# Performance work log

Hardware: AMD Instinct MI355X
Metric: run time of the kernel (lower is better)

Reference implementation:

```python
import jax, jax.numpy as jnp
import numpy as np

N_NODES = 100000
N_EDGES = 600000
IN_DIM = 128
OUT_DIM = 64


def setup_inputs() -> dict:
    key = jax.random.key(0)
    k1, k2, k3, k4, k5 = jax.random.split(key, 5)
    x = jax.random.normal(k1, (N_NODES, IN_DIM), dtype=jnp.float32)
    edge_index = jax.random.randint(k2, (2, N_EDGES), 0, N_NODES, dtype=jnp.int64)
    edge_weight = jax.random.uniform(k3, (N_EDGES,), dtype=jnp.float32)
    W1 = jax.random.normal(k4, (IN_DIM, IN_DIM), dtype=jnp.float32) / np.sqrt(IN_DIM)
    b1 = jnp.zeros((IN_DIM,), dtype=jnp.float32)
    W2 = jax.random.normal(k5, (IN_DIM, OUT_DIM), dtype=jnp.float32) / np.sqrt(IN_DIM)
    b2 = jnp.zeros((OUT_DIM,), dtype=jnp.float32)
    return {"x": x, "edge_index": edge_index, "edge_weight": edge_weight,
            "W1": W1, "b1": b1, "W2": W2, "b2": b2}


def _spmm(edge_index, edge_weight, h):
    # out[dst] = sum_{e: dst(e)=dst} w_e * h[src(e)]  -- normalized adjacency SpMM
    src, dst = edge_index[0], edge_index[1]
    msg = h[src] * edge_weight[:, None]          # [E, D] gather + scale
    return jax.ops.segment_sum(msg, dst, num_segments=h.shape[0])  # [N, D]


def reference(x, edge_index, edge_weight, W1, b1, W2, b2):
    # Layer 1: GCNConv(in,in) -> ReLU (dropout is identity in eval mode)
    h = _spmm(edge_index, edge_weight, x @ W1) + b1
    h = jax.nn.relu(h)
    # Layer 2: GCNConv(in,out)
    out = _spmm(edge_index, edge_weight, h @ W2) + b2
    return out
```

## Files before the change

kernel.cpp:

```cpp
#include <hip/hip_runtime.h>

#define NN 100000
#define NE 600000
#define DIN 128
#define DOUT 64
#define SCAN_B 256
#define NBLK ((NN + SCAN_B - 1) / SCAN_B)
#define HIST_B ((NE + 255) / 256)
#define PREP_N (DIN * DIN + DIN * DOUT)
#define PREP_B ((PREP_N + 255) / 256)

typedef __attribute__((ext_vector_type(8))) short bf16x8;
typedef __attribute__((ext_vector_type(4))) short s16x4;
typedef __attribute__((ext_vector_type(4))) float f32x4;

__device__ inline short f2bf(float f) {
  union { float f; unsigned u; } v; v.f = f;
  unsigned r = (v.u + 0x7FFF + ((v.u >> 16) & 1)) >> 16;
  return (short)r;
}
__device__ inline float bf2f(unsigned short u) {
  union { unsigned u; float f; } v; v.u = ((unsigned)u) << 16;
  return v.f;
}

__global__ __launch_bounds__(256) void hist_prep_kernel(const int* __restrict__ ei,
                                                        int* __restrict__ cnt,
                                                        const float* __restrict__ W1,
                                                        short* __restrict__ w1t,
                                                        const float* __restrict__ W2,
                                                        short* __restrict__ w2t) {
  const int b = blockIdx.x, t = threadIdx.x;
  if (b < HIST_B) {
    int e = b * 256 + t;
    if (e < NE) atomicAdd(&cnt[ei[NE + e]], 1);
  } else {
    int i = (b - HIST_B) * 256 + t;
    if (i < DIN * DIN) {
      int n = i >> 7, k = i & 127;
      w1t[i] = f2bf(W1[k * DIN + n]);
    } else if (i < PREP_N) {
      int i2 = i - DIN * DIN;
      int n = i2 >> 7, k = i2 & 127;
      w2t[i2] = f2bf(W2[k * DOUT + n]);
    }
  }
}

__global__ __launch_bounds__(256) void scan_local_kernel(const int* __restrict__ cnt,
                                                         int* __restrict__ row_ptr,
                                                         int* __restrict__ blk_sum) {
  __shared__ int s[256];
  const int b = blockIdx.x, t = threadIdx.x;
  const int i = b * 256 + t;
  int v = (i < NN) ? cnt[i] : 0;
  s[t] = v;
  __syncthreads();
  for (int off = 1; off < 256; off <<= 1) {
    int u = (t >= off) ? s[t - off] : 0;
    __syncthreads();
    s[t] += u;
    __syncthreads();
  }
  if (i < NN) row_ptr[i] = s[t] - v;
  if (t == 255) blk_sum[b] = s[255];
}

__global__ __launch_bounds__(512) void scan_blk_kernel(const int* __restrict__ blk_sum,
                                                       int* __restrict__ blk_off) {
  __shared__ int s[512];
  const int t = threadIdx.x;
  int v = (t < NBLK) ? blk_sum[t] : 0;
  s[t] = v;
  __syncthreads();
  for (int off = 1; off < 512; off <<= 1) {
    int u = (t >= off) ? s[t - off] : 0;
    __syncthreads();
    s[t] += u;
    __syncthreads();
  }
  if (t < NBLK) blk_off[t] = s[t] - v;
}

__global__ __launch_bounds__(256) void scan_add_kernel(int* __restrict__ row_ptr,
                                                       const int* __restrict__ blk_off,
                                                       int* __restrict__ next) {
  const int b = blockIdx.x, t = threadIdx.x;
  const int i = b * 256 + t;
  if (i < NN) {
    int v = row_ptr[i] + blk_off[b];
    row_ptr[i] = v;
    next[i] = v;
  }
  if (i == 0) row_ptr[NN] = NE;
}

__global__ __launch_bounds__(256) void scatter_kernel(const int* __restrict__ ei,
                                                      const float* __restrict__ ew,
                                                      int* __restrict__ next,
                                                      int2* __restrict__ ep) {
  int e = blockIdx.x * 256 + threadIdx.x;
  if (e >= NE) return;
  int src = ei[e];
  int dst = ei[NE + e];
  int pos = atomicAdd(&next[dst], 1);
  ep[pos] = make_int2(src, __float_as_int(ew[e]));
}

#define G1_BM 128
#define XS_PITCH 136
__global__ __launch_bounds__(256) void gemm1_mfma_kernel(const float* __restrict__ x,
                                                         const short* __restrict__ w1t,
                                                         short* __restrict__ h0) {
  __shared__ short xs[G1_BM][XS_PITCH];
  const int t = threadIdx.x;
  const int row0 = blockIdx.x * G1_BM;
#pragma unroll
  for (int i = 0; i < 16; ++i) {
    int f = t + i * 256;
    int r = f >> 5, c4 = f & 31;
    int gr = row0 + r;
    float4 v = (gr < NN) ? *(const float4*)&x[(size_t)gr * DIN + c4 * 4]
                         : make_float4(0.f, 0.f, 0.f, 0.f);
    s16x4 s;
    s.x = f2bf(v.x); s.y = f2bf(v.y); s.z = f2bf(v.z); s.w = f2bf(v.w);
    *(s16x4*)&xs[r][c4 * 4] = s;
  }
  __syncthreads();

  const int wave = t >> 6, lane = t & 63;
  const int nlane = lane & 15, quad = lane >> 4;
  const int mbase = wave * 32;
  f32x4 acc[2][8];
#pragma unroll
  for (int mt = 0; mt < 2; ++mt)
#pragma unroll
    for (int nt = 0; nt < 8; ++nt) acc[mt][nt] = (f32x4){0.f, 0.f, 0.f, 0.f};

#pragma unroll
  for (int ks = 0; ks < 4; ++ks) {
    const int koff = ks * 32 + quad * 8;
    bf16x8 a0 = *(const bf16x8*)&xs[mbase + nlane][koff];
    bf16x8 a1 = *(const bf16x8*)&xs[mbase + 16 + nlane][koff];
#pragma unroll
    for (int nt = 0; nt < 8; ++nt) {
      bf16x8 b = *(const bf16x8*)&w1t[(size_t)(nt * 16 + nlane) * DIN + koff];
      acc[0][nt] = __builtin_amdgcn_mfma_f32_16x16x32_bf16(a0, b, acc[0][nt], 0, 0, 0);
      acc[1][nt] = __builtin_amdgcn_mfma_f32_16x16x32_bf16(a1, b, acc[1][nt], 0, 0, 0);
    }
  }

#pragma unroll
  for (int mt = 0; mt < 2; ++mt)
#pragma unroll
    for (int nt = 0; nt < 8; ++nt)
#pragma unroll
      for (int rg = 0; rg < 4; ++rg) {
        int gr = row0 + mbase + mt * 16 + quad * 4 + rg;
        if (gr < NN) h0[(size_t)gr * DIN + nt * 16 + nlane] = f2bf(acc[mt][nt][rg]);
      }
}

__global__ __launch_bounds__(256) void gemm2_mfma_kernel(const short* __restrict__ acc1,
                                                         const float* __restrict__ b1,
                                                         const short* __restrict__ w2t,
                                                         short* __restrict__ h2) {
  __shared__ short xs[G1_BM][XS_PITCH];
  const int t = threadIdx.x;
  const int row0 = blockIdx.x * G1_BM;
#pragma unroll
  for (int i = 0; i < 8; ++i) {
    int f = t + i * 256;
    int r = f >> 4, c8 = f & 15;
    int gr = row0 + r;
    bf16x8 v = (gr < NN) ? *(const bf16x8*)&acc1[(size_t)gr * DIN + c8 * 8]
                         : (bf16x8){0, 0, 0, 0, 0, 0, 0, 0};
    bf16x8 s;
#pragma unroll
    for (int j = 0; j < 8; ++j) {
      float fv = bf2f((unsigned short)v[j]) + b1[c8 * 8 + j];
      s[j] = f2bf(fmaxf(fv, 0.f));
    }
    *(bf16x8*)&xs[r][c8 * 8] = s;
  }
  __syncthreads();

  const int wave = t >> 6, lane = t & 63;
  const int nlane = lane & 15, quad = lane >> 4;
  const int mbase = wave * 32;
  f32x4 acc[2][4];
#pragma unroll
  for (int mt = 0; mt < 2; ++mt)
#pragma unroll
    for (int nt = 0; nt < 4; ++nt) acc[mt][nt] = (f32x4){0.f, 0.f, 0.f, 0.f};

#pragma unroll
  for (int ks = 0; ks < 4; ++ks) {
    const int koff = ks * 32 + quad * 8;
    bf16x8 a0 = *(const bf16x8*)&xs[mbase + nlane][koff];
    bf16x8 a1 = *(const bf16x8*)&xs[mbase + 16 + nlane][koff];
#pragma unroll
    for (int nt = 0; nt < 4; ++nt) {
      bf16x8 b = *(const bf16x8*)&w2t[(size_t)(nt * 16 + nlane) * DIN + koff];
      acc[0][nt] = __builtin_amdgcn_mfma_f32_16x16x32_bf16(a0, b, acc[0][nt], 0, 0, 0);
      acc[1][nt] = __builtin_amdgcn_mfma_f32_16x16x32_bf16(a1, b, acc[1][nt], 0, 0, 0);
    }
  }

#pragma unroll
  for (int mt = 0; mt < 2; ++mt)
#pragma unroll
    for (int nt = 0; nt < 4; ++nt)
#pragma unroll
      for (int rg = 0; rg < 4; ++rg) {
        int gr = row0 + mbase + mt * 16 + quad * 4 + rg;
        if (gr < NN) h2[(size_t)gr * DOUT + nt * 16 + nlane] = f2bf(acc[mt][nt][rg]);
      }
}

template <int D, int LPE, bool BIAS, bool OUTBF>
__global__ __launch_bounds__(256) void spmm_gather_kernel(
    const int* __restrict__ rp, const int2* __restrict__ ep,
    const short* __restrict__ h, const float* __restrict__ bias,
    void* __restrict__ outv) {
  const int row = blockIdx.x * (256 / LPE) + threadIdx.x / LPE;
  const int lane = threadIdx.x % LPE;
  if (row >= NN) return;
  const int b = rp[row], e = rp[row + 1];
  float acc[8];
#pragma unroll
  for (int j = 0; j < 8; ++j) acc[j] = 0.f;
  int i = b;
  for (; i + 4 <= e; i += 4) {
    int2 p0 = ep[i], p1 = ep[i + 1], p2 = ep[i + 2], p3 = ep[i + 3];
    bf16x8 v0 = *(const bf16x8*)&h[(size_t)p0.x * D + lane * 8];
    bf16x8 v1 = *(const bf16x8*)&h[(size_t)p1.x * D + lane * 8];
    bf16x8 v2 = *(const bf16x8*)&h[(size_t)p2.x * D + lane * 8];
    bf16x8 v3 = *(const bf16x8*)&h[(size_t)p3.x * D + lane * 8];
    float w0 = __int_as_float(p0.y), w1 = __int_as_float(p1.y);
    float w2 = __int_as_float(p2.y), w3 = __int_as_float(p3.y);
#pragma unroll
    for (int j = 0; j < 8; ++j)
      acc[j] += w0 * bf2f((unsigned short)v0[j]) + w1 * bf2f((unsigned short)v1[j]) +
                w2 * bf2f((unsigned short)v2[j]) + w3 * bf2f((unsigned short)v3[j]);
  }
  if (i + 2 <= e) {
    int2 p0 = ep[i], p1 = ep[i + 1];
    bf16x8 v0 = *(const bf16x8*)&h[(size_t)p0.x * D + lane * 8];
    bf16x8 v1 = *(const bf16x8*)&h[(size_t)p1.x * D + lane * 8];
    float w0 = __int_as_float(p0.y), w1 = __int_as_float(p1.y);
#pragma unroll
    for (int j = 0; j < 8; ++j)
      acc[j] += w0 * bf2f((unsigned short)v0[j]) + w1 * bf2f((unsigned short)v1[j]);
    i += 2;
  }
  if (i < e) {
    int2 p0 = ep[i];
    bf16x8 v0 = *(const bf16x8*)&h[(size_t)p0.x * D + lane * 8];
    float w0 = __int_as_float(p0.y);
#pragma unroll
    for (int j = 0; j < 8; ++j) acc[j] += w0 * bf2f((unsigned short)v0[j]);
  }
  if (BIAS) {
#pragma unroll
    for (int j = 0; j < 8; ++j) acc[j] += bias[lane * 8 + j];
  }
  if (OUTBF) {
    bf16x8 o;
#pragma unroll
    for (int j = 0; j < 8; ++j) o[j] = f2bf(acc[j]);
    *(bf16x8*)((short*)outv + (size_t)row * D + lane * 8) = o;
  } else {
    float* out = (float*)outv;
    *(float4*)&out[(size_t)row * D + lane * 8] = make_float4(acc[0], acc[1], acc[2], acc[3]);
    *(float4*)&out[(size_t)row * D + lane * 8 + 4] = make_float4(acc[4], acc[5], acc[6], acc[7]);
  }
}

extern "C" void kernel_launch(void* const* d_in, const int* in_sizes, int n_in,
                              void* d_out, int out_size, void* d_ws, size_t ws_size,
                              hipStream_t stream) {
  const float* x  = (const float*)d_in[0];
  const int*   ei = (const int*)d_in[1];
  const float* ew = (const float*)d_in[2];
  const float* W1 = (const float*)d_in[3];
  const float* b1 = (const float*)d_in[4];
  const float* W2 = (const float*)d_in[5];
  const float* b2 = (const float*)d_in[6];
  float* out = (float*)d_out;

  char* p = (char*)d_ws;
  int*   cnt     = (int*)p;                 p += sizeof(int) * NN;
  int*   row_ptr = (int*)p;                 p += sizeof(int) * (NN + 4);
  int*   blk_sum = (int*)p;                 p += sizeof(int) * (NBLK + 1);
  int*   blk_off = (int*)p;                 p += sizeof(int) * (NBLK + 1);
  int2*  ep      = (int2*)p;                p += sizeof(int2) * NE;
  short* w1t     = (short*)p;               p += sizeof(short) * DIN * DIN;
  short* w2t     = (short*)p;               p += sizeof(short) * DIN * DOUT;
  short* h0      = (short*)p;               p += sizeof(short) * (size_t)NN * DIN;
  short* acc1    = (short*)p;
  int*   next    = cnt;
  short* h2      = h0;

  hipMemsetAsync(cnt, 0, sizeof(int) * NN, stream);
  hist_prep_kernel<<<HIST_B + PREP_B, 256, 0, stream>>>(ei, cnt, W1, w1t, W2, w2t);
  scan_local_kernel<<<NBLK, 256, 0, stream>>>(cnt, row_ptr, blk_sum);
  scan_blk_kernel<<<1, 512, 0, stream>>>(blk_sum, blk_off);
  scan_add_kernel<<<NBLK, 256, 0, stream>>>(row_ptr, blk_off, next);
  scatter_kernel<<<HIST_B, 256, 0, stream>>>(ei, ew, next, ep);

  gemm1_mfma_kernel<<<(NN + G1_BM - 1) / G1_BM, 256, 0, stream>>>(x, w1t, h0);
  spmm_gather_kernel<DIN, 16, false, true>
      <<<(NN * 16 + 255) / 256, 256, 0, stream>>>(row_ptr, ep, h0, nullptr, acc1);

  gemm2_mfma_kernel<<<(NN + G1_BM - 1) / G1_BM, 256, 0, stream>>>(acc1, b1, w2t, h2);
  spmm_gather_kernel<DOUT, 8, true, false>
      <<<(NN * 8 + 255) / 256, 256, 0, stream>>>(row_ptr, ep, h2, b2, out);
}
```

Measured before the change: 261.7 us.

## Store layer-1 features in fp8, record atomic ranks, and merge scan kernels

The first GEMM now writes its output as fp8 instead of bf16, and the first SpMM gathers 16 fp8 values per lane. This halves the bytes in the random-gather step. The histogram pass saves each edge's atomic rank so the scatter computes positions directly, with no second atomic pass. The three-kernel scan becomes two kernels of 512-thread blocks, each redoing the small block-sum scan. The fp8 storage adds substantial quantization error to the layer-1 intermediate, which may break accuracy tolerances.

```diff
diff --git a/kernel.cpp b/kernel.cpp
--- a/kernel.cpp
+++ b/kernel.cpp
@@ -4,7 +4,7 @@
 #define NE 600000
 #define DIN 128
 #define DOUT 64
-#define SCAN_B 256
+#define SCAN_B 512
 #define NBLK ((NN + SCAN_B - 1) / SCAN_B)
 #define HIST_B ((NE + 255) / 256)
 #define PREP_N (DIN * DIN + DIN * DOUT)
@@ -13,6 +13,7 @@
 typedef __attribute__((ext_vector_type(8))) short bf16x8;
 typedef __attribute__((ext_vector_type(4))) short s16x4;
 typedef __attribute__((ext_vector_type(4))) float f32x4;
+typedef __attribute__((ext_vector_type(2))) float f32x2;
 
 __device__ inline short f2bf(float f) {
   union { float f; unsigned u; } v; v.f = f;
@@ -23,9 +24,25 @@
   union { unsigned u; float f; } v; v.u = ((unsigned)u) << 16;
   return v.f;
 }
+__device__ inline unsigned char f2fp8(float f) {
+  unsigned pk = __builtin_amdgcn_cvt_pk_fp8_f32(f, f, 0, false);
+  return (unsigned char)(pk & 0xff);
+}
+__device__ inline void fma_fp8x16(uint4 q, float w, float* acc) {
+  f32x2 f;
+  f = __builtin_amdgcn_cvt_pk_f32_fp8(q.x, false); acc[0] += w * f[0];  acc[1] += w * f[1];
+  f = __builtin_amdgcn_cvt_pk_f32_fp8(q.x, true);  acc[2] += w * f[0];  acc[3] += w * f[1];
+  f = __builtin_amdgcn_cvt_pk_f32_fp8(q.y, false); acc[4] += w * f[0];  acc[5] += w * f[1];
+  f = __builtin_amdgcn_cvt_pk_f32_fp8(q.y, true);  acc[6] += w * f[0];  acc[7] += w * f[1];
+  f = __builtin_amdgcn_cvt_pk_f32_fp8(q.z, false); acc[8] += w * f[0];  acc[9] += w * f[1];
+  f = __builtin_amdgcn_cvt_pk_f32_fp8(q.z, true);  acc[10] += w * f[0]; acc[11] += w * f[1];
+  f = __builtin_amdgcn_cvt_pk_f32_fp8(q.w, false); acc[12] += w * f[0]; acc[13] += w * f[1];
+  f = __builtin_amdgcn_cvt_pk_f32_fp8(q.w, true);  acc[14] += w * f[0]; acc[15] += w * f[1];
+}
 
 __global__ __launch_bounds__(256) void hist_prep_kernel(const int* __restrict__ ei,
                                                         int* __restrict__ cnt,
+                                                        int* __restrict__ rank,
                                                         const float* __restrict__ W1,
                                                         short* __restrict__ w1t,
                                                         const float* __restrict__ W2,
@@ -33,7 +50,7 @@
   const int b = blockIdx.x, t = threadIdx.x;
   if (b < HIST_B) {
     int e = b * 256 + t;
-    if (e < NE) atomicAdd(&cnt[ei[NE + e]], 1);
+    if (e < NE) rank[e] = atomicAdd(&cnt[ei[NE + e]], 1);
   } else {
     int i = (b - HIST_B) * 256 + t;
     if (i < DIN * DIN) {
@@ -47,30 +64,13 @@
   }
 }
 
-__global__ __launch_bounds__(256) void scan_local_kernel(const int* __restrict__ cnt,
+__global__ __launch_bounds__(512) void scan_local_kernel(const int* __restrict__ cnt,
                                                          int* __restrict__ row_ptr,
                                                          int* __restrict__ blk_sum) {
-  __shared__ int s[256];
+  __shared__ int s[512];
   const int b = blockIdx.x, t = threadIdx.x;
-  const int i = b * 256 + t;
+  const int i = b * 512 + t;
   int v = (i < NN) ? cnt[i] : 0;
-  s[t] = v;
-  __syncthreads();
-  for (int off = 1; off < 256; off <<= 1) {
-    int u = (t >= off) ? s[t - off] : 0;
-    __syncthreads();
-    s[t] += u;
-    __syncthreads();
-  }
-  if (i < NN) row_ptr[i] = s[t] - v;
-  if (t == 255) blk_sum[b] = s[255];
-}
-
-__global__ __launch_bounds__(512) void scan_blk_kernel(const int* __restrict__ blk_sum,
-                                                       int* __restrict__ blk_off) {
-  __shared__ int s[512];
-  const int t = threadIdx.x;
-  int v = (t < NBLK) ? blk_sum[t] : 0;
   s[t] = v;
   __syncthreads();
   for (int off = 1; off < 512; off <<= 1) {
@@ -79,31 +79,38 @@
     s[t] += u;
     __syncthreads();
   }
-  if (t < NBLK) blk_off[t] = s[t] - v;
-}
-
-__global__ __launch_bounds__(256) void scan_add_kernel(int* __restrict__ row_ptr,
-                                                       const int* __restrict__ blk_off,
-                                                       int* __restrict__ next) {
+  if (i < NN) row_ptr[i] = s[t] - v;
+  if (t == 511) blk_sum[b] = s[511];
+}
+
+__global__ __launch_bounds__(512) void scan_add_kernel(int* __restrict__ row_ptr,
+                                                       const int* __restrict__ blk_sum) {
+  __shared__ int s[512];
   const int b = blockIdx.x, t = threadIdx.x;
-  const int i = b * 256 + t;
-  if (i < NN) {
-    int v = row_ptr[i] + blk_off[b];
-    row_ptr[i] = v;
-    next[i] = v;
-  }
-  if (i == 0) row_ptr[NN] = NE;
+  s[t] = (t < NBLK) ? blk_sum[t] : 0;
+  __syncthreads();
+  for (int off = 1; off < 512; off <<= 1) {
+    int u = (t >= off) ? s[t - off] : 0;
+    __syncthreads();
+    s[t] += u;
+    __syncthreads();
+  }
+  int off = (b > 0) ? s[b - 1] : 0;
+  const int i = b * 512 + t;
+  if (i < NN) row_ptr[i] += off;
+  if (b == 0 && t == 0) row_ptr[NN] = NE;
 }
 
 __global__ __launch_bounds__(256) void scatter_kernel(const int* __restrict__ ei,
                                                       const float* __restrict__ ew,
-                                                      int* __restrict__ next,
+                                                      const int* __restrict__ row_ptr,
+                                                      const int* __restrict__ rank,
                                                       int2* __restrict__ ep) {
   int e = blockIdx.x * 256 + threadIdx.x;
   if (e >= NE) return;
   int src = ei[e];
   int dst = ei[NE + e];
-  int pos = atomicAdd(&next[dst], 1);
+  int pos = row_ptr[dst] + rank[e];
   ep[pos] = make_int2(src, __float_as_int(ew[e]));
 }
 
@@ -111,7 +118,7 @@
 #define XS_PITCH 136
 __global__ __launch_bounds__(256) void gemm1_mfma_kernel(const float* __restrict__ x,
                                                          const short* __restrict__ w1t,
-                                                         short* __restrict__ h0) {
+                                                         unsigned char* __restrict__ h0) {
   __shared__ short xs[G1_BM][XS_PITCH];
   const int t = threadIdx.x;
   const int row0 = blockIdx.x * G1_BM;
@@ -157,7 +164,7 @@
 #pragma unroll
       for (int rg = 0; rg < 4; ++rg) {
         int gr = row0 + mbase + mt * 16 + quad * 4 + rg;
-        if (gr < NN) h0[(size_t)gr * DIN + nt * 16 + nlane] = f2bf(acc[mt][nt][rg]);
+        if (gr < NN) h0[(size_t)gr * DIN + nt * 16 + nlane] = f2fp8(acc[mt][nt][rg]);
       }
 }
 
@@ -218,13 +225,56 @@
       }
 }
 
-template <int D, int LPE, bool BIAS, bool OUTBF>
-__global__ __launch_bounds__(256) void spmm_gather_kernel(
-    const int* __restrict__ rp, const int2* __restrict__ ep,
-    const short* __restrict__ h, const float* __restrict__ bias,
-    void* __restrict__ outv) {
-  const int row = blockIdx.x * (256 / LPE) + threadIdx.x / LPE;
-  const int lane = threadIdx.x % LPE;
+__global__ __launch_bounds__(256) void spmm1_fp8_kernel(const int* __restrict__ rp,
+                                                        const int2* __restrict__ ep,
+                                                        const unsigned char* __restrict__ h,
+                                                        short* __restrict__ acc1) {
+  const int row = blockIdx.x * 32 + (threadIdx.x >> 3);
+  const int lane = threadIdx.x & 7;
+  if (row >= NN) return;
+  const int b = rp[row], e = rp[row + 1];
+  float acc[16];
+#pragma unroll
+  for (int j = 0; j < 16; ++j) acc[j] = 0.f;
+  int i = b;
+  for (; i + 4 <= e; i += 4) {
+    int2 p0 = ep[i], p1 = ep[i + 1], p2 = ep[i + 2], p3 = ep[i + 3];
+    uint4 q0 = *(const uint4*)&h[(size_t)p0.x * DIN + lane * 16];
+    uint4 q1 = *(const uint4*)&h[(size_t)p1.x * DIN + lane * 16];
+    uint4 q2 = *(const uint4*)&h[(size_t)p2.x * DIN + lane * 16];
+    uint4 q3 = *(const uint4*)&h[(size_t)p3.x * DIN + lane * 16];
+    fma_fp8x16(q0, __int_as_float(p0.y), acc);
+    fma_fp8x16(q1, __int_as_float(p1.y), acc);
+    fma_fp8x16(q2, __int_as_float(p2.y), acc);
+    fma_fp8x16(q3, __int_as_float(p3.y), acc);
+  }
+  if (i + 2 <= e) {
+    int2 p0 = ep[i], p1 = ep[i + 1];
+    uint4 q0 = *(const uint4*)&h[(size_t)p0.x * DIN + lane * 16];
+    uint4 q1 = *(const uint4*)&h[(size_t)p1.x * DIN + lane * 16];
+    fma_fp8x16(q0, __int_as_float(p0.y), acc);
+    fma_fp8x16(q1, __int_as_float(p1.y), acc);
+    i += 2;
+  }
+  if (i < e) {
+    int2 p0 = ep[i];
+    uint4 q0 = *(const uint4*)&h[(size_t)p0.x * DIN + lane * 16];
+    fma_fp8x16(q0, __int_as_float(p0.y), acc);
+  }
+  bf16x8 o0, o1;
+#pragma unroll
+  for (int j = 0; j < 8; ++j) { o0[j] = f2bf(acc[j]); o1[j] = f2bf(acc[8 + j]); }
+  *(bf16x8*)&acc1[(size_t)row * DIN + lane * 16] = o0;
+  *(bf16x8*)&acc1[(size_t)row * DIN + lane * 16 + 8] = o1;
+}
+
+__global__ __launch_bounds__(256) void spmm2_kernel(const int* __restrict__ rp,
+                                                    const int2* __restrict__ ep,
+                                                    const short* __restrict__ h,
+                                                    const float* __restrict__ bias,
+                                                    float* __restrict__ out) {
+  const int row = blockIdx.x * 32 + (threadIdx.x >> 3);
+  const int lane = threadIdx.x & 7;
   if (row >= NN) return;
   const int b = rp[row], e = rp[row + 1];
   float acc[8];
@@ -233,10 +283,10 @@
   int i = b;
   for (; i + 4 <= e; i += 4) {
     int2 p0 = ep[i], p1 = ep[i + 1], p2 = ep[i + 2], p3 = ep[i + 3];
-    bf16x8 v0 = *(const bf16x8*)&h[(size_t)p0.x * D + lane * 8];
-    bf16x8 v1 = *(const bf16x8*)&h[(size_t)p1.x * D + lane * 8];
-    bf16x8 v2 = *(const bf16x8*)&h[(size_t)p2.x * D + lane * 8];
-    bf16x8 v3 = *(const bf16x8*)&h[(size_t)p3.x * D + lane * 8];
+    bf16x8 v0 = *(const bf16x8*)&h[(size_t)p0.x * DOUT + lane * 8];
+    bf16x8 v1 = *(const bf16x8*)&h[(size_t)p1.x * DOUT + lane * 8];
+    bf16x8 v2 = *(const bf16x8*)&h[(size_t)p2.x * DOUT + lane * 8];
+    bf16x8 v3 = *(const bf16x8*)&h[(size_t)p3.x * DOUT + lane * 8];
     float w0 = __int_as_float(p0.y), w1 = __int_as_float(p1.y);
     float w2 = __int_as_float(p2.y), w3 = __int_as_float(p3.y);
 #pragma unroll
@@ -246,8 +296,8 @@
   }
   if (i + 2 <= e) {
     int2 p0 = ep[i], p1 = ep[i + 1];
-    bf16x8 v0 = *(const bf16x8*)&h[(size_t)p0.x * D + lane * 8];
-    bf16x8 v1 = *(const bf16x8*)&h[(size_t)p1.x * D + lane * 8];
+    bf16x8 v0 = *(const bf16x8*)&h[(size_t)p0.x * DOUT + lane * 8];
+    bf16x8 v1 = *(const bf16x8*)&h[(size_t)p1.x * DOUT + lane * 8];
     float w0 = __int_as_float(p0.y), w1 = __int_as_float(p1.y);
 #pragma unroll
     for (int j = 0; j < 8; ++j)
@@ -256,25 +306,15 @@
   }
   if (i < e) {
     int2 p0 = ep[i];
-    bf16x8 v0 = *(const bf16x8*)&h[(size_t)p0.x * D + lane * 8];
+    bf16x8 v0 = *(const bf16x8*)&h[(size_t)p0.x * DOUT + lane * 8];
     float w0 = __int_as_float(p0.y);
 #pragma unroll
     for (int j = 0; j < 8; ++j) acc[j] += w0 * bf2f((unsigned short)v0[j]);
   }
-  if (BIAS) {
-#pragma unroll
-    for (int j = 0; j < 8; ++j) acc[j] += bias[lane * 8 + j];
-  }
-  if (OUTBF) {
-    bf16x8 o;
-#pragma unroll
-    for (int j = 0; j < 8; ++j) o[j] = f2bf(acc[j]);
-    *(bf16x8*)((short*)outv + (size_t)row * D + lane * 8) = o;
-  } else {
-    float* out = (float*)outv;
-    *(float4*)&out[(size_t)row * D + lane * 8] = make_float4(acc[0], acc[1], acc[2], acc[3]);
-    *(float4*)&out[(size_t)row * D + lane * 8 + 4] = make_float4(acc[4], acc[5], acc[6], acc[7]);
-  }
+#pragma unroll
+  for (int j = 0; j < 8; ++j) acc[j] += bias[lane * 8 + j];
+  *(float4*)&out[(size_t)row * DOUT + lane * 8] = make_float4(acc[0], acc[1], acc[2], acc[3]);
+  *(float4*)&out[(size_t)row * DOUT + lane * 8 + 4] = make_float4(acc[4], acc[5], acc[6], acc[7]);
 }
 
 extern "C" void kernel_launch(void* const* d_in, const int* in_sizes, int n_in,
@@ -292,28 +332,24 @@
   char* p = (char*)d_ws;
   int*   cnt     = (int*)p;                 p += sizeof(int) * NN;
   int*   row_ptr = (int*)p;                 p += sizeof(int) * (NN + 4);
-  int*   blk_sum = (int*)p;                 p += sizeof(int) * (NBLK + 1);
-  int*   blk_off = (int*)p;                 p += sizeof(int) * (NBLK + 1);
+  int*   blk_sum = (int*)p;                 p += sizeof(int) * (NBLK + 4);
+  int*   rank    = (int*)p;                 p += sizeof(int) * NE;
   int2*  ep      = (int2*)p;                p += sizeof(int2) * NE;
   short* w1t     = (short*)p;               p += sizeof(short) * DIN * DIN;
   short* w2t     = (short*)p;               p += sizeof(short) * DIN * DOUT;
-  short* h0      = (short*)p;               p += sizeof(short) * (size_t)NN * DIN;
+  unsigned char* h0 = (unsigned char*)p;    p += (size_t)NN * DIN;
   short* acc1    = (short*)p;
-  int*   next    = cnt;
-  short* h2      = h0;
+  short* h2      = (short*)h0;
 
   hipMemsetAsync(cnt, 0, sizeof(int) * NN, stream);
-  hist_prep_kernel<<<HIST_B + PREP_B, 256, 0, stream>>>(ei, cnt, W1, w1t, W2, w2t);
-  scan_local_kernel<<<NBLK, 256, 0, stream>>>(cnt, row_ptr, blk_sum);
-  scan_blk_kernel<<<1, 512, 0, stream>>>(blk_sum, blk_off);
-  scan_add_kernel<<<NBLK, 256, 0, stream>>>(row_ptr, blk_off, next);
-  scatter_kernel<<<HIST_B, 256, 0, stream>>>(ei, ew, next, ep);
+  hist_prep_kernel<<<HIST_B + PREP_B, 256, 0, stream>>>(ei, cnt, rank, W1, w1t, W2, w2t);
+  scan_local_kernel<<<NBLK, 512, 0, stream>>>(cnt, row_ptr, blk_sum);
+  scan_add_kernel<<<NBLK, 512, 0, stream>>>(row_ptr, blk_sum);
+  scatter_kernel<<<HIST_B, 256, 0, stream>>>(ei, ew, row_ptr, rank, ep);
 
   gemm1_mfma_kernel<<<(NN + G1_BM - 1) / G1_BM, 256, 0, stream>>>(x, w1t, h0);
-  spmm_gather_kernel<DIN, 16, false, true>
-      <<<(NN * 16 + 255) / 256, 256, 0, stream>>>(row_ptr, ep, h0, nullptr, acc1);
+  spmm1_fp8_kernel<<<(NN + 31) / 32, 256, 0, stream>>>(row_ptr, ep, h0, acc1);
 
   gemm2_mfma_kernel<<<(NN + G1_BM - 1) / G1_BM, 256, 0, stream>>>(acc1, b1, w2t, h2);
-  spmm_gather_kernel<DOUT, 8, true, false>
-      <<<(NN * 8 + 255) / 256, 256, 0, stream>>>(row_ptr, ep, h2, b2, out);
-}
+  spmm2_kernel<<<(NN + 31) / 32, 256, 0, stream>>>(row_ptr, ep, h2, b2, out);
+}
```

Result: faster. 235.3 us (-10.1%).
